# Kernel optimization log

Measured on AMD Instinct MI355X. Metric: run time of the kernel, lower is better.

The kernel has to match this reference:

```python
import jax, jax.numpy as jnp
import numpy as np

N_HEAD, DK, DV = 16, 64, 64
TEMP = DK ** 0.5
LN_EPS = 1e-5


def setup_inputs() -> dict:
    key = jax.random.key(0)
    ks = jax.random.split(key, 8)
    B, LQ, LK = 8, 1024, 1024
    D1, D2 = 768, 1024
    return {
        'q': jax.random.normal(ks[0], (B, LQ, D1), jnp.float32),
        'k': jax.random.normal(ks[1], (B, LK, D2), jnp.float32),
        'v': jax.random.normal(ks[2], (B, LK, D2), jnp.float32),
        'w_qs': jax.random.normal(ks[3], (D1, N_HEAD * DK), jnp.float32) * 0.02,
        'w_ks': jax.random.normal(ks[4], (D2, N_HEAD * DK), jnp.float32) * 0.02,
        'w_vs': jax.random.normal(ks[5], (D2, N_HEAD * DV), jnp.float32) * 0.02,
        'fc_w': jax.random.normal(ks[6], (N_HEAD * DV, D2), jnp.float32) * 0.02,
        'resid_w': jax.random.normal(ks[7], (D1, N_HEAD * DV), jnp.float32) * 0.02,
        'resid_b': jnp.zeros((N_HEAD * DV,), jnp.float32),
        'ln_gamma': jnp.ones((D2,), jnp.float32),
        'ln_beta': jnp.zeros((D2,), jnp.float32),
    }


def reference(q, k, v, w_qs, w_ks, w_vs, fc_w, resid_w, resid_b, ln_gamma, ln_beta):
    B, LQ, _ = q.shape
    LK = k.shape[1]
    residual = q
    # project and split heads: [B, L, H, d] -> [B, H, L, d]
    Q = (q @ w_qs).reshape(B, LQ, N_HEAD, DK).transpose(0, 2, 1, 3)
    K = (k @ w_ks).reshape(B, LK, N_HEAD, DK).transpose(0, 2, 1, 3)
    V = (v @ w_vs).reshape(B, LK, N_HEAD, DV).transpose(0, 2, 1, 3)
    scores = jnp.einsum('bhqd,bhkd->bhqk', Q / TEMP, K)
    p = jax.nn.softmax(scores, axis=-1)
    # reverse-complement attention (RCA): reverse=True
    p = (1.0 - p) / (LK - 1)
    out = jnp.einsum('bhqk,bhkd->bhqd', p, V)  # dropout is eval-mode identity
    out = out.transpose(0, 2, 1, 3).reshape(B, LQ, N_HEAD * DV)
    out = out @ fc_w
    out = out + (residual @ resid_w + resid_b)
    mean = jnp.mean(out, axis=-1, keepdims=True)
    var = jnp.var(out, axis=-1, keepdims=True)
    out = (out - mean) * jax.lax.rsqrt(var + LN_EPS) * ln_gamma + ln_beta
    return out  # relu=False
```

## Files before the change

kernel.cpp:

```cpp
#include <hip/hip_runtime.h>

typedef __bf16 bf16_t;
typedef __bf16 bf16x8 __attribute__((ext_vector_type(8)));
typedef __bf16 bf16x4 __attribute__((ext_vector_type(4)));
typedef float  f32x4  __attribute__((ext_vector_type(4)));

#if __has_builtin(__builtin_amdgcn_exp2f)
#define EXP2(x) __builtin_amdgcn_exp2f(x)
#else
#define EXP2(x) exp2f(x)
#endif

#define DEVFN __device__ __forceinline__

DEVFN void gl_lds16(void* lds_base, const void* gsrc) {
  __builtin_amdgcn_global_load_lds(
      (const __attribute__((address_space(1))) void*)gsrc,
      (__attribute__((address_space(3))) void*)lds_base, 16, 0, 0);
}

__global__ __launch_bounds__(256) void k_prep(
    const float* __restrict__ q, const float* __restrict__ k, const float* __restrict__ v,
    const float* __restrict__ w_qs, const float* __restrict__ w_ks,
    const float* __restrict__ w_vs, const float* __restrict__ fc_w,
    const float* __restrict__ resid_w,
    bf16_t* __restrict__ qb, bf16_t* __restrict__ kb, bf16_t* __restrict__ vb,
    bf16_t* __restrict__ wqsT, bf16_t* __restrict__ wksT, bf16_t* __restrict__ wvsT,
    bf16_t* __restrict__ fcwT, bf16_t* __restrict__ rswT,
    float* __restrict__ Vs) {
  __shared__ float t[64][65];
  int bid = blockIdx.x;
  if (bid < 1152) {
    const float* w; bf16_t* wt; int K;
    if (bid < 192)      { w = w_qs;    wt = wqsT; K = 768; }
    else if (bid < 448) { w = w_ks;    wt = wksT; K = 1024; bid -= 192; }
    else if (bid < 704) { w = w_vs;    wt = wvsT; K = 1024; bid -= 448; }
    else if (bid < 960) { w = fc_w;    wt = fcwT; K = 1024; bid -= 704; }
    else                { w = resid_w; wt = rswT; K = 768;  bid -= 960; }
    const int bk = (bid >> 4) << 6;
    const int bn = (bid & 15) << 6;
    const int rr = threadIdx.x >> 4;
    const int cc = (threadIdx.x & 15) << 2;
#pragma unroll
    for (int i = 0; i < 4; ++i) {
      int r = i * 16 + rr;
      float4 vv = *reinterpret_cast<const float4*>(&w[(size_t)(bk + r) * 1024 + bn + cc]);
      t[r][cc] = vv.x; t[r][cc + 1] = vv.y; t[r][cc + 2] = vv.z; t[r][cc + 3] = vv.w;
    }
    __syncthreads();
#pragma unroll
    for (int i = 0; i < 4; ++i) {
      int n = i * 16 + rr;
      bf16x4 o;
      o[0] = (bf16_t)t[cc][n];     o[1] = (bf16_t)t[cc + 1][n];
      o[2] = (bf16_t)t[cc + 2][n]; o[3] = (bf16_t)t[cc + 3][n];
      *reinterpret_cast<bf16x4*>(&wt[(size_t)(bn + n) * K + bk + cc]) = o;
    }
    return;
  }
  bid -= 1152;
  if (bid == 0) {
    for (int j = threadIdx.x; j < 8192; j += 256) Vs[j] = 0.f;
  }
  const int NQ = 1572864, NK = 2097152, NT = NQ + 2 * NK;
  int stride = (gridDim.x - 1152) * 256;
  for (int i = bid * 256 + threadIdx.x; i < NT; i += stride) {
    const float* src; bf16_t* dst; int off;
    if (i < NQ)           { src = q; dst = qb; off = i; }
    else if (i < NQ + NK) { src = k; dst = kb; off = i - NQ; }
    else                  { src = v; dst = vb; off = i - NQ - NK; }
    float4 vv = reinterpret_cast<const float4*>(src)[off];
    bf16x4 o;
    o[0] = (bf16_t)vv.x; o[1] = (bf16_t)vv.y; o[2] = (bf16_t)vv.z; o[3] = (bf16_t)vv.w;
    reinterpret_cast<bf16x4*>(dst)[off] = o;
  }
}

__global__ __launch_bounds__(256) void k_transpose_v(
    const bf16_t* __restrict__ Vp, bf16_t* __restrict__ Vt, float* __restrict__ Vs) {
  const int kt = blockIdx.x & 15;
  const int bh = blockIdx.x >> 4;
  const int b = bh >> 4, h = bh & 15;
  __shared__ unsigned short t[64][72];
  __shared__ float red[4][64];
#pragma unroll
  for (int i = 0; i < 2; ++i) {
    int cid = i * 256 + threadIdx.x;
    int r = cid >> 3, c = (cid & 7) * 8;
    uint4 v = *reinterpret_cast<const uint4*>(
        Vp + ((size_t)(b * 1024 + kt * 64 + r)) * 1024 + h * 64 + c);
    const unsigned short* pv = reinterpret_cast<const unsigned short*>(&v);
#pragma unroll
    for (int j = 0; j < 8; ++j) t[r][c + j] = pv[j];
  }
  __syncthreads();
#pragma unroll
  for (int i = 0; i < 2; ++i) {
    int cid = i * 256 + threadIdx.x;
    int d = cid >> 3, c = (cid & 7) * 8;
    unsigned short tmp[8];
#pragma unroll
    for (int j = 0; j < 8; ++j) tmp[j] = t[c + j][d];
    char* dst = (char*)Vt + ((size_t)(bh * 16 + kt)) * 8192 + d * 128 +
                ((((c >> 3) ^ (d & 7))) << 4);
    *reinterpret_cast<uint4*>(dst) = *reinterpret_cast<uint4*>(tmp);
  }
  const int d = threadIdx.x & 63, seg = threadIdx.x >> 6;
  float s = 0.f;
#pragma unroll
  for (int i = 0; i < 16; ++i)
    s += (float)*(const bf16_t*)&t[seg * 16 + i][d];
  red[seg][d] = s;
  __syncthreads();
  if (threadIdx.x < 64)
    atomicAdd(&Vs[bh * 64 + threadIdx.x],
              red[0][threadIdx.x] + red[1][threadIdx.x] + red[2][threadIdx.x] + red[3][threadIdx.x]);
}

DEVFN void gemm_core(const bf16_t* __restrict__ A, const bf16_t* __restrict__ Bt,
                     bf16_t* __restrict__ C, int N, int K, float oscale,
                     int wg, bf16_t (*sm)[4096]) {
  const int tn = N >> 7;
  const int m0 = (wg / tn) << 7;
  const int n0 = (wg % tn) << 7;
  const int lane = threadIdx.x & 63;
  const int wv = threadIdx.x >> 6;
  const int wr = (wv >> 1) * 64, wc = (wv & 1) * 64;
  const int lr = lane & 15, lk = lane >> 4;
  const int so0 = wv * 2048 + lane * 16;
  const int so1 = so0 + 1024;
  const int r0 = so0 >> 6, r1 = so1 >> 6;
  const int c0 = ((((so0 >> 4) & 3) ^ (r0 & 3)) << 4);
  const int c1 = ((((so1 >> 4) & 3) ^ (r1 & 3)) << 4);
  const int asw = ((lk ^ (lr & 3)) << 4);
  const char* Apc = (const char*)A;
  const char* Btc = (const char*)Bt;
  f32x4 zro = {0.f, 0.f, 0.f, 0.f};
  f32x4 acc[4][4];
#pragma unroll
  for (int i = 0; i < 4; ++i)
#pragma unroll
    for (int j = 0; j < 4; ++j) acc[i][j] = zro;

  const int nk = K >> 5;
  auto stage = [&](int buf, int t) {
    gl_lds16((char*)sm[buf] + wv * 2048,        Apc + ((size_t)(m0 + r0) * K + t * 32) * 2 + c0);
    gl_lds16((char*)sm[buf] + wv * 2048 + 1024, Apc + ((size_t)(m0 + r1) * K + t * 32) * 2 + c1);
    gl_lds16((char*)sm[2 + buf] + wv * 2048,        Btc + ((size_t)(n0 + r0) * K + t * 32) * 2 + c0);
    gl_lds16((char*)sm[2 + buf] + wv * 2048 + 1024, Btc + ((size_t)(n0 + r1) * K + t * 32) * 2 + c1);
  };
  stage(0, 0);
  __syncthreads();
  for (int t = 0; t < nk; ++t) {
    const int cur = t & 1;
    if (t + 1 < nk) stage(cur ^ 1, t + 1);
    const char* AsB = (const char*)sm[cur];
    const char* BsB = (const char*)sm[2 + cur];
    bf16x8 af[4], bfr[4];
#pragma unroll
    for (int i = 0; i < 4; ++i)
      af[i] = *(const bf16x8*)(AsB + (wr + i * 16 + lr) * 64 + asw);
#pragma unroll
    for (int j = 0; j < 4; ++j)
      bfr[j] = *(const bf16x8*)(BsB + (wc + j * 16 + lr) * 64 + asw);
#pragma unroll
    for (int i = 0; i < 4; ++i)
#pragma unroll
      for (int j = 0; j < 4; ++j)
        acc[i][j] = __builtin_amdgcn_mfma_f32_16x16x32_bf16(af[i], bfr[j], acc[i][j], 0, 0, 0);
    __syncthreads();
  }
#pragma unroll
  for (int i = 0; i < 4; ++i)
#pragma unroll
    for (int j = 0; j < 4; ++j)
#pragma unroll
      for (int r = 0; r < 4; ++r)
        C[(size_t)(m0 + wr + i * 16 + lk * 4 + r) * N + n0 + wc + j * 16 + lr] =
            (bf16_t)(acc[i][j][r] * oscale);
}

__global__ __launch_bounds__(256) void k_gemm_proj(
    const bf16_t* __restrict__ qb, const bf16_t* __restrict__ wqsT, bf16_t* __restrict__ Qp,
    const bf16_t* __restrict__ kb, const bf16_t* __restrict__ wksT, bf16_t* __restrict__ Kp,
    const bf16_t* __restrict__ vb, const bf16_t* __restrict__ wvsT, bf16_t* __restrict__ Vp,
    float qscale) {
  __shared__ bf16_t sm[4][4096];
  const int bid = blockIdx.x;
  const int route = bid >> 9;
  const int sbid = bid & 511;
  const int wg = (sbid & 7) * 64 + (sbid >> 3);
  if (route == 0)      gemm_core(qb, wqsT, Qp, 1024, 768,  qscale, wg, sm);
  else if (route == 1) gemm_core(kb, wksT, Kp, 1024, 1024, 1.0f,   wg, sm);
  else                 gemm_core(vb, wvsT, Vp, 1024, 1024, 1.0f,   wg, sm);
}

__global__ __launch_bounds__(256) void k_gemm_final(
    const bf16_t* __restrict__ A1, const bf16_t* __restrict__ B1t, int K1,
    const bf16_t* __restrict__ A2, const bf16_t* __restrict__ B2t, int K2,
    const float* __restrict__ bias, bf16_t* __restrict__ Y, int N) {
  __shared__ bf16_t sm[4][4096];
  const int bpx = gridDim.x >> 3;
  const int wg = (blockIdx.x & 7) * bpx + (blockIdx.x >> 3);
  const int tn = N >> 7;
  const int m0 = (wg / tn) << 7;
  const int n0 = (wg % tn) << 7;
  const int lane = threadIdx.x & 63;
  const int wv = threadIdx.x >> 6;
  const int wr = (wv >> 1) * 64, wc = (wv & 1) * 64;
  const int lr = lane & 15, lk = lane >> 4;
  const int so0 = wv * 2048 + lane * 16;
  const int so1 = so0 + 1024;
  const int r0 = so0 >> 6, r1 = so1 >> 6;
  const int c0 = ((((so0 >> 4) & 3) ^ (r0 & 3)) << 4);
  const int c1 = ((((so1 >> 4) & 3) ^ (r1 & 3)) << 4);
  const int asw = ((lk ^ (lr & 3)) << 4);
  f32x4 zro = {0.f, 0.f, 0.f, 0.f};
  f32x4 acc[4][4];
#pragma unroll
  for (int i = 0; i < 4; ++i)
#pragma unroll
    for (int j = 0; j < 4; ++j) acc[i][j] = zro;

  const bf16_t* Ap[2] = {A1, A2};
  const bf16_t* Bp[2] = {B1t, B2t};
  const int Kp_[2] = {K1, K2};
  for (int ph = 0; ph < 2; ++ph) {
    const char* Apc = (const char*)Ap[ph];
    const char* Btc = (const char*)Bp[ph];
    const int K = Kp_[ph];
    const int nk = K >> 5;
    auto stage = [&](int buf, int t) {
      gl_lds16((char*)sm[buf] + wv * 2048,        Apc + ((size_t)(m0 + r0) * K + t * 32) * 2 + c0);
      gl_lds16((char*)sm[buf] + wv * 2048 + 1024, Apc + ((size_t)(m0 + r1) * K + t * 32) * 2 + c1);
      gl_lds16((char*)sm[2 + buf] + wv * 2048,        Btc + ((size_t)(n0 + r0) * K + t * 32) * 2 + c0);
      gl_lds16((char*)sm[2 + buf] + wv * 2048 + 1024, Btc + ((size_t)(n0 + r1) * K + t * 32) * 2 + c1);
    };
    stage(0, 0);
    __syncthreads();
    for (int t = 0; t < nk; ++t) {
      const int cur = t & 1;
      if (t + 1 < nk) stage(cur ^ 1, t + 1);
      const char* AsB = (const char*)sm[cur];
      const char* BsB = (const char*)sm[2 + cur];
      bf16x8 af[4], bfr[4];
#pragma unroll
      for (int i = 0; i < 4; ++i)
        af[i] = *(const bf16x8*)(AsB + (wr + i * 16 + lr) * 64 + asw);
#pragma unroll
      for (int j = 0; j < 4; ++j)
        bfr[j] = *(const bf16x8*)(BsB + (wc + j * 16 + lr) * 64 + asw);
#pragma unroll
      for (int i = 0; i < 4; ++i)
#pragma unroll
        for (int j = 0; j < 4; ++j)
          acc[i][j] = __builtin_amdgcn_mfma_f32_16x16x32_bf16(af[i], bfr[j], acc[i][j], 0, 0, 0);
      __syncthreads();
    }
  }
#pragma unroll
  for (int i = 0; i < 4; ++i)
#pragma unroll
    for (int j = 0; j < 4; ++j) {
      float bv = bias[n0 + wc + j * 16 + lr];
#pragma unroll
      for (int r = 0; r < 4; ++r)
        Y[(size_t)(m0 + wr + i * 16 + lk * 4 + r) * N + n0 + wc + j * 16 + lr] =
            (bf16_t)(acc[i][j][r] + bv);
    }
}

__global__ __launch_bounds__(256) void k_attn(
    const bf16_t* __restrict__ Qp, const bf16_t* __restrict__ Kp,
    const bf16_t* __restrict__ Vt, const float* __restrict__ Vsum,
    bf16_t* __restrict__ Aout) {
  const int bid = blockIdx.x;
  const int wgid = (bid & 7) * 128 + (bid >> 3);
  const int qg = wgid & 7;
  const int bh = wgid >> 3;
  const int b = bh >> 4, h = bh & 15;
  __shared__ bf16_t Ks[2][64 * 64];
  __shared__ bf16_t Vs[2][64 * 64];
  const int lane = threadIdx.x & 63;
  const int wv = threadIdx.x >> 6;
  const int lr = lane & 15, lk = lane >> 4;

  const int o0 = wv * 2048 + lane * 16;
  const int o1 = o0 + 1024;
  const int row0 = o0 >> 7, row1 = o1 >> 7;
  const int sc0 = ((((o0 >> 4) & 7) ^ (row0 & 7)) << 4);
  const int sc1 = ((((o1 >> 4) & 7) ^ (row1 & 7)) << 4);
  const int srow0 = (row0 & 0x23) | ((row0 & 0x0C) << 1) | ((row0 & 0x10) >> 2);
  const int srow1 = (row1 & 0x23) | ((row1 & 0x0C) << 1) | ((row1 & 0x10) >> 2);

  const char* Ksrc0 = (const char*)(Kp + ((size_t)(b * 1024 + srow0)) * 1024 + h * 64) + sc0;
  const char* Ksrc1 = (const char*)(Kp + ((size_t)(b * 1024 + srow1)) * 1024 + h * 64) + sc1;
  const char* Vtile = (const char*)Vt + (size_t)bh * 131072 + o0;

  gl_lds16((char*)&Ks[0][0] + o0, Ksrc0);
  gl_lds16((char*)&Ks[0][0] + o1, Ksrc1);
  gl_lds16((char*)&Vs[0][0] + o0, Vtile);
  gl_lds16((char*)&Vs[0][0] + o1, Vtile + 1024);

  bf16x8 qa[2][2];
#pragma unroll
  for (int st = 0; st < 2; ++st) {
    const char* qsrc =
        (const char*)(Qp + ((size_t)(b * 1024 + qg * 128 + st * 64 + wv * 16 + lr)) * 1024 + h * 64);
    qa[st][0] = *(const bf16x8*)(qsrc + lk * 16);
    qa[st][1] = *(const bf16x8*)(qsrc + 64 + lk * 16);
  }
  __syncthreads();

  const int kb0 = lr * 128 + ((lk ^ (lr & 7)) << 4);
  const int kb1 = lr * 128 + (((4 + lk) ^ (lr & 7)) << 4);
  const int vsw0 = lr * 128 + (((0 + lk) ^ (lr & 7)) << 4);
  const int vsw1 = lr * 128 + (((4 + lk) ^ (lr & 7)) << 4);

  f32x4 zro = {0.f, 0.f, 0.f, 0.f};
  f32x4 oacc[2][4];
  f32x4 sum[2];
#pragma unroll
  for (int st = 0; st < 2; ++st) {
    sum[st] = zro;
#pragma unroll
    for (int g = 0; g < 4; ++g) oacc[st][g] = zro;
  }
  bf16x8 ones8;
#pragma unroll
  for (int j = 0; j < 8; ++j) ones8[j] = (bf16_t)1.0f;

  for (int kt = 0; kt < 16; ++kt) {
    const int cur = kt & 1;
    const char* KsB = (const char*)&Ks[cur][0];
    const char* VsB = (const char*)&Vs[cur][0];
    if (kt < 15) {
      char* KsN = (char*)&Ks[cur ^ 1][0];
      char* VsN = (char*)&Vs[cur ^ 1][0];
      const size_t koff = (size_t)(kt + 1) * 131072;
      const size_t voff = (size_t)(kt + 1) * 8192;
      gl_lds16(KsN + o0, Ksrc0 + koff);
      gl_lds16(KsN + o1, Ksrc1 + koff);
      gl_lds16(VsN + o0, Vtile + voff);
      gl_lds16(VsN + o1, Vtile + voff + 1024);
    }

    f32x4 sacc[2][4];
#pragma unroll
    for (int st = 0; st < 2; ++st)
#pragma unroll
      for (int g = 0; g < 4; ++g) sacc[st][g] = zro;
    {
      bf16x8 kf[4];
#pragma unroll
      for (int g = 0; g < 4; ++g) kf[g] = *(const bf16x8*)(KsB + kb0 + g * 2048);
#pragma unroll
      for (int st = 0; st < 2; ++st)
#pragma unroll
        for (int g = 0; g < 4; ++g)
          sacc[st][g] = __builtin_amdgcn_mfma_f32_16x16x32_bf16(kf[g], qa[st][0], sacc[st][g], 0, 0, 0);
#pragma unroll
      for (int g = 0; g < 4; ++g) kf[g] = *(const bf16x8*)(KsB + kb1 + g * 2048);
#pragma unroll
      for (int st = 0; st < 2; ++st)
#pragma unroll
        for (int g = 0; g < 4; ++g)
          sacc[st][g] = __builtin_amdgcn_mfma_f32_16x16x32_bf16(kf[g], qa[st][1], sacc[st][g], 0, 0, 0);
    }

    bf16x8 pa[2][2];
#pragma unroll
    for (int st = 0; st < 2; ++st)
#pragma unroll
      for (int c = 0; c < 2; ++c) {
        bf16x8 pw;
#pragma unroll
        for (int r = 0; r < 4; ++r) {
          pw[r]     = (bf16_t)EXP2(sacc[st][2 * c][r]);
          pw[4 + r] = (bf16_t)EXP2(sacc[st][2 * c + 1][r]);
        }
        pa[st][c] = pw;
      }

#pragma unroll
    for (int c = 0; c < 2; ++c) {
      const int vb = (c == 0) ? vsw0 : vsw1;
      bf16x8 vf[4];
#pragma unroll
      for (int gd = 0; gd < 4; ++gd)
        vf[gd] = *(const bf16x8*)(VsB + vb + gd * 2048);
#pragma unroll
      for (int st = 0; st < 2; ++st) {
        sum[st] = __builtin_amdgcn_mfma_f32_16x16x32_bf16(pa[st][c], ones8, sum[st], 0, 0, 0);
#pragma unroll
        for (int gd = 0; gd < 4; ++gd)
          oacc[st][gd] = __builtin_amdgcn_mfma_f32_16x16x32_bf16(pa[st][c], vf[gd], oacc[st][gd], 0, 0, 0);
      }
    }
    __syncthreads();
  }

  float vs_d[4];
#pragma unroll
  for (int gd = 0; gd < 4; ++gd) vs_d[gd] = Vsum[bh * 64 + gd * 16 + lr];
#pragma unroll
  for (int st = 0; st < 2; ++st) {
    float inv[4];
#pragma unroll
    for (int r = 0; r < 4; ++r) inv[r] = 1.0f / sum[st][r];
#pragma unroll
    for (int gd = 0; gd < 4; ++gd)
#pragma unroll
      for (int r = 0; r < 4; ++r) {
        int d = gd * 16 + lr;
        int qrow = qg * 128 + st * 64 + wv * 16 + lk * 4 + r;
        float attnv = oacc[st][gd][r] * inv[r];
        float val = (vs_d[gd] - attnv) * (1.0f / 1023.0f);
        Aout[((size_t)(b * 1024 + qrow)) * 1024 + h * 64 + d] = (bf16_t)val;
      }
  }
}

__global__ __launch_bounds__(256) void k_ln(
    const bf16_t* __restrict__ Y, const float* __restrict__ gamma,
    const float* __restrict__ beta, float* __restrict__ out) {
  const int row = blockIdx.x, tid = threadIdx.x;
  bf16x4 xv = reinterpret_cast<const bf16x4*>(Y + (size_t)row * 1024)[tid];
  float x0 = (float)xv[0], x1 = (float)xv[1], x2 = (float)xv[2], x3 = (float)xv[3];
  float s = x0 + x1 + x2 + x3;
  float q = x0 * x0 + x1 * x1 + x2 * x2 + x3 * x3;
#pragma unroll
  for (int off = 32; off > 0; off >>= 1) {
    s += __shfl_xor(s, off, 64);
    q += __shfl_xor(q, off, 64);
  }
  __shared__ float ss[4], qs[4];
  if ((tid & 63) == 0) { ss[tid >> 6] = s; qs[tid >> 6] = q; }
  __syncthreads();
  s = ss[0] + ss[1] + ss[2] + ss[3];
  q = qs[0] + qs[1] + qs[2] + qs[3];
  float mean = s * (1.f / 1024.f);
  float var = q * (1.f / 1024.f) - mean * mean;
  float rstd = rsqrtf(var + 1e-5f);
  float4 g = reinterpret_cast<const float4*>(gamma)[tid];
  float4 bt = reinterpret_cast<const float4*>(beta)[tid];
  float4 o;
  o.x = (x0 - mean) * rstd * g.x + bt.x;
  o.y = (x1 - mean) * rstd * g.y + bt.y;
  o.z = (x2 - mean) * rstd * g.z + bt.z;
  o.w = (x3 - mean) * rstd * g.w + bt.w;
  reinterpret_cast<float4*>(out + (size_t)row * 1024)[tid] = o;
}

extern "C" void kernel_launch(void* const* d_in, const int* in_sizes, int n_in,
                              void* d_out, int out_size, void* d_ws, size_t ws_size,
                              hipStream_t stream) {
  (void)in_sizes; (void)n_in; (void)out_size;
  const float* q       = (const float*)d_in[0];
  const float* k       = (const float*)d_in[1];
  const float* v       = (const float*)d_in[2];
  const float* w_qs    = (const float*)d_in[3];
  const float* w_ks    = (const float*)d_in[4];
  const float* w_vs    = (const float*)d_in[5];
  const float* fc_w    = (const float*)d_in[6];
  const float* resid_w = (const float*)d_in[7];
  const float* resid_b = (const float*)d_in[8];
  const float* ln_g    = (const float*)d_in[9];
  const float* ln_b    = (const float*)d_in[10];
  float* out = (float*)d_out;
  char* ws = (char*)d_ws;

  if (ws_size < (size_t)122716160) return;

  bf16_t* qb   = (bf16_t*)(ws + 0);
  bf16_t* kb   = (bf16_t*)(ws + 12582912);
  bf16_t* vb   = (bf16_t*)(ws + 29360128);
  bf16_t* Y    = (bf16_t*)(ws + 12582912);
  bf16_t* wqsT = (bf16_t*)(ws + 46137344);
  bf16_t* wksT = (bf16_t*)(ws + 47710208);
  bf16_t* wvsT = (bf16_t*)(ws + 49807360);
  bf16_t* fcwT = (bf16_t*)(ws + 51904512);
  bf16_t* rswT = (bf16_t*)(ws + 54001664);
  bf16_t* Qp   = (bf16_t*)(ws + 55574528);
  bf16_t* Kp   = (bf16_t*)(ws + 72351744);
  bf16_t* Vp   = (bf16_t*)(ws + 89128960);
  bf16_t* Aout = (bf16_t*)(ws + 89128960);
  bf16_t* VtT  = (bf16_t*)(ws + 105906176);
  float*  Vsm  = (float*)(ws + 122683392);

  k_prep<<<3200, 256, 0, stream>>>(q, k, v, w_qs, w_ks, w_vs, fc_w, resid_w,
                                   qb, kb, vb, wqsT, wksT, wvsT, fcwT, rswT, Vsm);
  k_gemm_proj<<<1536, 256, 0, stream>>>(qb, wqsT, Qp, kb, wksT, Kp, vb, wvsT, Vp,
                                        0.18033688011f);
  k_transpose_v<<<2048, 256, 0, stream>>>(Vp, VtT, Vsm);
  k_attn<<<1024, 256, 0, stream>>>(Qp, Kp, VtT, Vsm, Aout);
  k_gemm_final<<<512, 256, 0, stream>>>(Aout, fcwT, 1024, qb, rswT, 768, resid_b, Y, 1024);
  k_ln<<<8192, 256, 0, stream>>>(Y, ln_g, ln_b, out);
}
```

Measured before the change: 195.4 us.

## Fuse V transpose and column sums into projection GEMM epilogue; widen attention blocks

The V projection GEMM now writes its output straight into the swizzled transposed tile layout that attention expects, and accumulates per-head column sums with atomics. This removes the separate transpose kernel along with its extra write and read of the V projection. The attention kernel moves to 512-thread blocks covering 256 query rows, so each staged K/V tile is shared by twice as many waves and the grid is halved. The final GEMM is refactored to call a shared tile routine with two accumulators, which raises register pressure.

```diff
diff --git a/kernel.cpp b/kernel.cpp
--- a/kernel.cpp
+++ b/kernel.cpp
@@ -76,53 +76,8 @@
   }
 }
 
-__global__ __launch_bounds__(256) void k_transpose_v(
-    const bf16_t* __restrict__ Vp, bf16_t* __restrict__ Vt, float* __restrict__ Vs) {
-  const int kt = blockIdx.x & 15;
-  const int bh = blockIdx.x >> 4;
-  const int b = bh >> 4, h = bh & 15;
-  __shared__ unsigned short t[64][72];
-  __shared__ float red[4][64];
-#pragma unroll
-  for (int i = 0; i < 2; ++i) {
-    int cid = i * 256 + threadIdx.x;
-    int r = cid >> 3, c = (cid & 7) * 8;
-    uint4 v = *reinterpret_cast<const uint4*>(
-        Vp + ((size_t)(b * 1024 + kt * 64 + r)) * 1024 + h * 64 + c);
-    const unsigned short* pv = reinterpret_cast<const unsigned short*>(&v);
-#pragma unroll
-    for (int j = 0; j < 8; ++j) t[r][c + j] = pv[j];
-  }
-  __syncthreads();
-#pragma unroll
-  for (int i = 0; i < 2; ++i) {
-    int cid = i * 256 + threadIdx.x;
-    int d = cid >> 3, c = (cid & 7) * 8;
-    unsigned short tmp[8];
-#pragma unroll
-    for (int j = 0; j < 8; ++j) tmp[j] = t[c + j][d];
-    char* dst = (char*)Vt + ((size_t)(bh * 16 + kt)) * 8192 + d * 128 +
-                ((((c >> 3) ^ (d & 7))) << 4);
-    *reinterpret_cast<uint4*>(dst) = *reinterpret_cast<uint4*>(tmp);
-  }
-  const int d = threadIdx.x & 63, seg = threadIdx.x >> 6;
-  float s = 0.f;
-#pragma unroll
-  for (int i = 0; i < 16; ++i)
-    s += (float)*(const bf16_t*)&t[seg * 16 + i][d];
-  red[seg][d] = s;
-  __syncthreads();
-  if (threadIdx.x < 64)
-    atomicAdd(&Vs[bh * 64 + threadIdx.x],
-              red[0][threadIdx.x] + red[1][threadIdx.x] + red[2][threadIdx.x] + red[3][threadIdx.x]);
-}
-
-DEVFN void gemm_core(const bf16_t* __restrict__ A, const bf16_t* __restrict__ Bt,
-                     bf16_t* __restrict__ C, int N, int K, float oscale,
-                     int wg, bf16_t (*sm)[4096]) {
-  const int tn = N >> 7;
-  const int m0 = (wg / tn) << 7;
-  const int n0 = (wg % tn) << 7;
+DEVFN void gemm_tiles(const bf16_t* __restrict__ A, const bf16_t* __restrict__ Bt,
+                      int K, int m0, int n0, bf16_t (*sm)[4096], f32x4 (&acc)[4][4]) {
   const int lane = threadIdx.x & 63;
   const int wv = threadIdx.x >> 6;
   const int wr = (wv >> 1) * 64, wc = (wv & 1) * 64;
@@ -136,7 +91,6 @@
   const char* Apc = (const char*)A;
   const char* Btc = (const char*)Bt;
   f32x4 zro = {0.f, 0.f, 0.f, 0.f};
-  f32x4 acc[4][4];
 #pragma unroll
   for (int i = 0; i < 4; ++i)
 #pragma unroll
@@ -170,29 +124,81 @@
         acc[i][j] = __builtin_amdgcn_mfma_f32_16x16x32_bf16(af[i], bfr[j], acc[i][j], 0, 0, 0);
     __syncthreads();
   }
-#pragma unroll
-  for (int i = 0; i < 4; ++i)
-#pragma unroll
-    for (int j = 0; j < 4; ++j)
-#pragma unroll
-      for (int r = 0; r < 4; ++r)
-        C[(size_t)(m0 + wr + i * 16 + lk * 4 + r) * N + n0 + wc + j * 16 + lr] =
-            (bf16_t)(acc[i][j][r] * oscale);
 }
 
 __global__ __launch_bounds__(256) void k_gemm_proj(
     const bf16_t* __restrict__ qb, const bf16_t* __restrict__ wqsT, bf16_t* __restrict__ Qp,
     const bf16_t* __restrict__ kb, const bf16_t* __restrict__ wksT, bf16_t* __restrict__ Kp,
-    const bf16_t* __restrict__ vb, const bf16_t* __restrict__ wvsT, bf16_t* __restrict__ Vp,
-    float qscale) {
+    const bf16_t* __restrict__ vb, const bf16_t* __restrict__ wvsT, bf16_t* __restrict__ Vt,
+    float* __restrict__ Vsum, float qscale) {
   __shared__ bf16_t sm[4][4096];
   const int bid = blockIdx.x;
   const int route = bid >> 9;
   const int sbid = bid & 511;
   const int wg = (sbid & 7) * 64 + (sbid >> 3);
-  if (route == 0)      gemm_core(qb, wqsT, Qp, 1024, 768,  qscale, wg, sm);
-  else if (route == 1) gemm_core(kb, wksT, Kp, 1024, 1024, 1.0f,   wg, sm);
-  else                 gemm_core(vb, wvsT, Vp, 1024, 1024, 1.0f,   wg, sm);
+  const int tn = 8;
+  const int m0 = (wg / tn) << 7;
+  const int n0 = (wg % tn) << 7;
+  const int lane = threadIdx.x & 63;
+  const int wv = threadIdx.x >> 6;
+  const int wr = (wv >> 1) * 64, wc = (wv & 1) * 64;
+  const int lr = lane & 15, lk = lane >> 4;
+  f32x4 acc[4][4];
+
+  if (route == 0) {
+    gemm_tiles(qb, wqsT, 768, m0, n0, sm, acc);
+#pragma unroll
+    for (int i = 0; i < 4; ++i)
+#pragma unroll
+      for (int j = 0; j < 4; ++j)
+#pragma unroll
+        for (int r = 0; r < 4; ++r)
+          Qp[(size_t)(m0 + wr + i * 16 + lk * 4 + r) * 1024 + n0 + wc + j * 16 + lr] =
+              (bf16_t)(acc[i][j][r] * qscale);
+  } else if (route == 1) {
+    gemm_tiles(kb, wksT, 1024, m0, n0, sm, acc);
+#pragma unroll
+    for (int i = 0; i < 4; ++i)
+#pragma unroll
+      for (int j = 0; j < 4; ++j)
+#pragma unroll
+        for (int r = 0; r < 4; ++r)
+          Kp[(size_t)(m0 + wr + i * 16 + lk * 4 + r) * 1024 + n0 + wc + j * 16 + lr] =
+              (bf16_t)acc[i][j][r];
+  } else {
+    gemm_tiles(vb, wvsT, 1024, m0, n0, sm, acc);
+    const int b = m0 >> 10;
+    const int h = (n0 + wc) >> 6;
+    const int kt = ((m0 & 1023) + wr) >> 6;
+    const size_t tbase = (size_t)(b * 16 + h) * 131072 + (size_t)kt * 8192;
+#pragma unroll
+    for (int i = 0; i < 4; ++i) {
+      const int kvl = i * 16 + lk * 4;
+      const int csel = kvl >> 3;
+      const int hoff = (kvl & 7) * 2;
+#pragma unroll
+      for (int j = 0; j < 4; ++j) {
+        const int d = j * 16 + lr;
+        bf16x4 pw;
+#pragma unroll
+        for (int r = 0; r < 4; ++r) pw[r] = (bf16_t)acc[i][j][r];
+        char* dst = (char*)Vt + tbase + d * 128 + ((csel ^ (d & 7)) << 4) + hoff;
+        *reinterpret_cast<bf16x4*>(dst) = pw;
+      }
+    }
+#pragma unroll
+    for (int j = 0; j < 4; ++j) {
+      float s = 0.f;
+#pragma unroll
+      for (int i = 0; i < 4; ++i)
+#pragma unroll
+        for (int r = 0; r < 4; ++r) s += acc[i][j][r];
+      s += __shfl_xor(s, 16, 64);
+      s += __shfl_xor(s, 32, 64);
+      if (lane < 16)
+        atomicAdd(&Vsum[(b * 16 + h) * 64 + j * 16 + lane], s);
+    }
+  }
 }
 
 __global__ __launch_bounds__(256) void k_gemm_final(
@@ -209,55 +215,11 @@
   const int wv = threadIdx.x >> 6;
   const int wr = (wv >> 1) * 64, wc = (wv & 1) * 64;
   const int lr = lane & 15, lk = lane >> 4;
-  const int so0 = wv * 2048 + lane * 16;
-  const int so1 = so0 + 1024;
-  const int r0 = so0 >> 6, r1 = so1 >> 6;
-  const int c0 = ((((so0 >> 4) & 3) ^ (r0 & 3)) << 4);
-  const int c1 = ((((so1 >> 4) & 3) ^ (r1 & 3)) << 4);
-  const int asw = ((lk ^ (lr & 3)) << 4);
-  f32x4 zro = {0.f, 0.f, 0.f, 0.f};
   f32x4 acc[4][4];
-#pragma unroll
-  for (int i = 0; i < 4; ++i)
-#pragma unroll
-    for (int j = 0; j < 4; ++j) acc[i][j] = zro;
-
-  const bf16_t* Ap[2] = {A1, A2};
-  const bf16_t* Bp[2] = {B1t, B2t};
-  const int Kp_[2] = {K1, K2};
-  for (int ph = 0; ph < 2; ++ph) {
-    const char* Apc = (const char*)Ap[ph];
-    const char* Btc = (const char*)Bp[ph];
-    const int K = Kp_[ph];
-    const int nk = K >> 5;
-    auto stage = [&](int buf, int t) {
-      gl_lds16((char*)sm[buf] + wv * 2048,        Apc + ((size_t)(m0 + r0) * K + t * 32) * 2 + c0);
-      gl_lds16((char*)sm[buf] + wv * 2048 + 1024, Apc + ((size_t)(m0 + r1) * K + t * 32) * 2 + c1);
-      gl_lds16((char*)sm[2 + buf] + wv * 2048,        Btc + ((size_t)(n0 + r0) * K + t * 32) * 2 + c0);
-      gl_lds16((char*)sm[2 + buf] + wv * 2048 + 1024, Btc + ((size_t)(n0 + r1) * K + t * 32) * 2 + c1);
-    };
-    stage(0, 0);
-    __syncthreads();
-    for (int t = 0; t < nk; ++t) {
-      const int cur = t & 1;
-      if (t + 1 < nk) stage(cur ^ 1, t + 1);
-      const char* AsB = (const char*)sm[cur];
-      const char* BsB = (const char*)sm[2 + cur];
-      bf16x8 af[4], bfr[4];
-#pragma unroll
-      for (int i = 0; i < 4; ++i)
-        af[i] = *(const bf16x8*)(AsB + (wr + i * 16 + lr) * 64 + asw);
-#pragma unroll
-      for (int j = 0; j < 4; ++j)
-        bfr[j] = *(const bf16x8*)(BsB + (wc + j * 16 + lr) * 64 + asw);
-#pragma unroll
-      for (int i = 0; i < 4; ++i)
-#pragma unroll
-        for (int j = 0; j < 4; ++j)
-          acc[i][j] = __builtin_amdgcn_mfma_f32_16x16x32_bf16(af[i], bfr[j], acc[i][j], 0, 0, 0);
-      __syncthreads();
-    }
-  }
+  f32x4 acc2[4][4];
+  gemm_tiles(A1, B1t, K1, m0, n0, sm, acc);
+  __syncthreads();
+  gemm_tiles(A2, B2t, K2, m0, n0, sm, acc2);
 #pragma unroll
   for (int i = 0; i < 4; ++i)
 #pragma unroll
@@ -266,65 +228,62 @@
 #pragma unroll
       for (int r = 0; r < 4; ++r)
         Y[(size_t)(m0 + wr + i * 16 + lk * 4 + r) * N + n0 + wc + j * 16 + lr] =
-            (bf16_t)(acc[i][j][r] + bv);
-    }
-}
-
-__global__ __launch_bounds__(256) void k_attn(
+            (bf16_t)(acc[i][j][r] + acc2[i][j][r] + bv);
+    }
+}
+
+__global__ __launch_bounds__(512) void k_attn(
     const bf16_t* __restrict__ Qp, const bf16_t* __restrict__ Kp,
     const bf16_t* __restrict__ Vt, const float* __restrict__ Vsum,
     bf16_t* __restrict__ Aout) {
   const int bid = blockIdx.x;
-  const int wgid = (bid & 7) * 128 + (bid >> 3);
-  const int qg = wgid & 7;
-  const int bh = wgid >> 3;
+  const int wgid = (bid & 7) * 64 + (bid >> 3);
+  const int qg = wgid & 3;
+  const int bh = wgid >> 2;
   const int b = bh >> 4, h = bh & 15;
-  __shared__ bf16_t Ks[2][64 * 64];
-  __shared__ bf16_t Vs[2][64 * 64];
-  const int lane = threadIdx.x & 63;
-  const int wv = threadIdx.x >> 6;
+  __shared__ bf16_t Ks[2][4096];
+  __shared__ bf16_t Vs[2][4096];
+  const int tid = threadIdx.x;
+  const int lane = tid & 63;
+  const int wv = tid >> 6;
   const int lr = lane & 15, lk = lane >> 4;
-
-  const int o0 = wv * 2048 + lane * 16;
-  const int o1 = o0 + 1024;
-  const int row0 = o0 >> 7, row1 = o1 >> 7;
-  const int sc0 = ((((o0 >> 4) & 7) ^ (row0 & 7)) << 4);
-  const int sc1 = ((((o1 >> 4) & 7) ^ (row1 & 7)) << 4);
-  const int srow0 = (row0 & 0x23) | ((row0 & 0x0C) << 1) | ((row0 & 0x10) >> 2);
-  const int srow1 = (row1 & 0x23) | ((row1 & 0x0C) << 1) | ((row1 & 0x10) >> 2);
-
-  const char* Ksrc0 = (const char*)(Kp + ((size_t)(b * 1024 + srow0)) * 1024 + h * 64) + sc0;
-  const char* Ksrc1 = (const char*)(Kp + ((size_t)(b * 1024 + srow1)) * 1024 + h * 64) + sc1;
-  const char* Vtile = (const char*)Vt + (size_t)bh * 131072 + o0;
-
-  gl_lds16((char*)&Ks[0][0] + o0, Ksrc0);
-  gl_lds16((char*)&Ks[0][0] + o1, Ksrc1);
-  gl_lds16((char*)&Vs[0][0] + o0, Vtile);
-  gl_lds16((char*)&Vs[0][0] + o1, Vtile + 1024);
+  const int stb = (wv >> 2) * 2;
+  const int wrow = (wv & 3) * 16;
+
+  const int o = tid * 16;
+  const int row = o >> 7;
+  const int sc = ((((o >> 4) & 7) ^ (row & 7)) << 4);
+  const int srow = (row & 0x23) | ((row & 0x0C) << 1) | ((row & 0x10) >> 2);
+
+  const char* Ksrc  = (const char*)(Kp + ((size_t)(b * 1024 + srow)) * 1024 + h * 64) + sc;
+  const char* Vtile = (const char*)Vt + (size_t)bh * 131072 + o;
+
+  gl_lds16((char*)&Ks[0][0] + o, Ksrc);
+  gl_lds16((char*)&Vs[0][0] + o, Vtile);
 
   bf16x8 qa[2][2];
 #pragma unroll
-  for (int st = 0; st < 2; ++st) {
-    const char* qsrc =
-        (const char*)(Qp + ((size_t)(b * 1024 + qg * 128 + st * 64 + wv * 16 + lr)) * 1024 + h * 64);
-    qa[st][0] = *(const bf16x8*)(qsrc + lk * 16);
-    qa[st][1] = *(const bf16x8*)(qsrc + 64 + lk * 16);
+  for (int stl = 0; stl < 2; ++stl) {
+    const char* qsrc = (const char*)(Qp +
+        ((size_t)(b * 1024 + qg * 256 + (stb + stl) * 64 + wrow + lr)) * 1024 + h * 64);
+    qa[stl][0] = *(const bf16x8*)(qsrc + lk * 16);
+    qa[stl][1] = *(const bf16x8*)(qsrc + 64 + lk * 16);
   }
   __syncthreads();
 
   const int kb0 = lr * 128 + ((lk ^ (lr & 7)) << 4);
   const int kb1 = lr * 128 + (((4 + lk) ^ (lr & 7)) << 4);
-  const int vsw0 = lr * 128 + (((0 + lk) ^ (lr & 7)) << 4);
-  const int vsw1 = lr * 128 + (((4 + lk) ^ (lr & 7)) << 4);
+  const int vsw0 = kb0;
+  const int vsw1 = kb1;
 
   f32x4 zro = {0.f, 0.f, 0.f, 0.f};
   f32x4 oacc[2][4];
   f32x4 sum[2];
 #pragma unroll
-  for (int st = 0; st < 2; ++st) {
-    sum[st] = zro;
-#pragma unroll
-    for (int g = 0; g < 4; ++g) oacc[st][g] = zro;
+  for (int stl = 0; stl < 2; ++stl) {
+    sum[stl] = zro;
+#pragma unroll
+    for (int g = 0; g < 4; ++g) oacc[stl][g] = zro;
   }
   bf16x8 ones8;
 #pragma unroll
@@ -335,51 +294,45 @@
     const char* KsB = (const char*)&Ks[cur][0];
     const char* VsB = (const char*)&Vs[cur][0];
     if (kt < 15) {
-      char* KsN = (char*)&Ks[cur ^ 1][0];
-      char* VsN = (char*)&Vs[cur ^ 1][0];
-      const size_t koff = (size_t)(kt + 1) * 131072;
-      const size_t voff = (size_t)(kt + 1) * 8192;
-      gl_lds16(KsN + o0, Ksrc0 + koff);
-      gl_lds16(KsN + o1, Ksrc1 + koff);
-      gl_lds16(VsN + o0, Vtile + voff);
-      gl_lds16(VsN + o1, Vtile + voff + 1024);
+      gl_lds16((char*)&Ks[cur ^ 1][0] + o, Ksrc + (size_t)(kt + 1) * 131072);
+      gl_lds16((char*)&Vs[cur ^ 1][0] + o, Vtile + (size_t)(kt + 1) * 8192);
     }
 
     f32x4 sacc[2][4];
 #pragma unroll
-    for (int st = 0; st < 2; ++st)
-#pragma unroll
-      for (int g = 0; g < 4; ++g) sacc[st][g] = zro;
+    for (int stl = 0; stl < 2; ++stl)
+#pragma unroll
+      for (int g = 0; g < 4; ++g) sacc[stl][g] = zro;
     {
       bf16x8 kf[4];
 #pragma unroll
       for (int g = 0; g < 4; ++g) kf[g] = *(const bf16x8*)(KsB + kb0 + g * 2048);
 #pragma unroll
-      for (int st = 0; st < 2; ++st)
+      for (int stl = 0; stl < 2; ++stl)
 #pragma unroll
         for (int g = 0; g < 4; ++g)
-          sacc[st][g] = __builtin_amdgcn_mfma_f32_16x16x32_bf16(kf[g], qa[st][0], sacc[st][g], 0, 0, 0);
+          sacc[stl][g] = __builtin_amdgcn_mfma_f32_16x16x32_bf16(kf[g], qa[stl][0], sacc[stl][g], 0, 0, 0);
 #pragma unroll
       for (int g = 0; g < 4; ++g) kf[g] = *(const bf16x8*)(KsB + kb1 + g * 2048);
 #pragma unroll
-      for (int st = 0; st < 2; ++st)
+      for (int stl = 0; stl < 2; ++stl)
 #pragma unroll
         for (int g = 0; g < 4; ++g)
-          sacc[st][g] = __builtin_amdgcn_mfma_f32_16x16x32_bf16(kf[g], qa[st][1], sacc[st][g], 0, 0, 0);
+          sacc[stl][g] = __builtin_amdgcn_mfma_f32_16x16x32_bf16(kf[g], qa[stl][1], sacc[stl][g], 0, 0, 0);
     }
 
     bf16x8 pa[2][2];
 #pragma unroll
-    for (int st = 0; st < 2; ++st)
+    for (int stl = 0; stl < 2; ++stl)
 #pragma unroll
       for (int c = 0; c < 2; ++c) {
         bf16x8 pw;
 #pragma unroll
         for (int r = 0; r < 4; ++r) {
-          pw[r]     = (bf16_t)EXP2(sacc[st][2 * c][r]);
-          pw[4 + r] = (bf16_t)EXP2(sacc[st][2 * c + 1][r]);
+          pw[r]     = (bf16_t)EXP2(sacc[stl][2 * c][r]);
+          pw[4 + r] = (bf16_t)EXP2(sacc[stl][2 * c + 1][r]);
         }
-        pa[st][c] = pw;
+        pa[stl][c] = pw;
       }
 
 #pragma unroll
@@ -390,11 +343,11 @@
       for (int gd = 0; gd < 4; ++gd)
         vf[gd] = *(const bf16x8*)(VsB + vb + gd * 2048);
 #pragma unroll
-      for (int st = 0; st < 2; ++st) {
-        sum[st] = __builtin_amdgcn_mfma_f32_16x16x32_bf16(pa[st][c], ones8, sum[st], 0, 0, 0);
+      for (int stl = 0; stl < 2; ++stl) {
+        sum[stl] = __builtin_amdgcn_mfma_f32_16x16x32_bf16(pa[stl][c], ones8, sum[stl], 0, 0, 0);
 #pragma unroll
         for (int gd = 0; gd < 4; ++gd)
-          oacc[st][gd] = __builtin_amdgcn_mfma_f32_16x16x32_bf16(pa[st][c], vf[gd], oacc[st][gd], 0, 0, 0);
+          oacc[stl][gd] = __builtin_amdgcn_mfma_f32_16x16x32_bf16(pa[stl][c], vf[gd], oacc[stl][gd], 0, 0, 0);
       }
     }
     __syncthreads();
@@ -404,17 +357,17 @@
 #pragma unroll
   for (int gd = 0; gd < 4; ++gd) vs_d[gd] = Vsum[bh * 64 + gd * 16 + lr];
 #pragma unroll
-  for (int st = 0; st < 2; ++st) {
+  for (int stl = 0; stl < 2; ++stl) {
     float inv[4];
 #pragma unroll
-    for (int r = 0; r < 4; ++r) inv[r] = 1.0f / sum[st][r];
+    for (int r = 0; r < 4; ++r) inv[r] = 1.0f / sum[stl][r];
 #pragma unroll
     for (int gd = 0; gd < 4; ++gd)
 #pragma unroll
       for (int r = 0; r < 4; ++r) {
         int d = gd * 16 + lr;
-        int qrow = qg * 128 + st * 64 + wv * 16 + lk * 4 + r;
-        float attnv = oacc[st][gd][r] * inv[r];
+        int qrow = qg * 256 + (stb + stl) * 64 + wrow + lk * 4 + r;
+        float attnv = oacc[stl][gd][r] * inv[r];
         float val = (vs_d[gd] - attnv) * (1.0f / 1023.0f);
         Aout[((size_t)(b * 1024 + qrow)) * 1024 + h * 64 + d] = (bf16_t)val;
       }
@@ -483,17 +436,15 @@
   bf16_t* rswT = (bf16_t*)(ws + 54001664);
   bf16_t* Qp   = (bf16_t*)(ws + 55574528);
   bf16_t* Kp   = (bf16_t*)(ws + 72351744);
-  bf16_t* Vp   = (bf16_t*)(ws + 89128960);
   bf16_t* Aout = (bf16_t*)(ws + 89128960);
   bf16_t* VtT  = (bf16_t*)(ws + 105906176);
   float*  Vsm  = (float*)(ws + 122683392);
 
   k_prep<<<3200, 256, 0, stream>>>(q, k, v, w_qs, w_ks, w_vs, fc_w, resid_w,
                                    qb, kb, vb, wqsT, wksT, wvsT, fcwT, rswT, Vsm);
-  k_gemm_proj<<<1536, 256, 0, stream>>>(qb, wqsT, Qp, kb, wksT, Kp, vb, wvsT, Vp,
-                                        0.18033688011f);
-  k_transpose_v<<<2048, 256, 0, stream>>>(Vp, VtT, Vsm);
-  k_attn<<<1024, 256, 0, stream>>>(Qp, Kp, VtT, Vsm, Aout);
+  k_gemm_proj<<<1536, 256, 0, stream>>>(qb, wqsT, Qp, kb, wksT, Kp, vb, wvsT, VtT,
+                                        Vsm, 0.18033688011f);
+  k_attn<<<512, 512, 0, stream>>>(Qp, Kp, VtT, Vsm, Aout);
   k_gemm_final<<<512, 256, 0, stream>>>(Aout, fcwT, 1024, qb, rswT, 768, resid_b, Y, 1024);
   k_ln<<<8192, 256, 0, stream>>>(Y, ln_g, ln_b, out);
 }
```

Measured after the change: 178.8 us. -8.5%, faster.
